# Kernel optimization log

Hardware: AMD Instinct MI355X
Metric: run time of the kernel (lower is better)

Reference implementation:

```python
import jax, jax.numpy as jnp
import numpy as np

B, T, C = 2, 4096, 1024
H = 16            # n_head (== n_groups == n_kv_heads)
HD = C // H       # head_dim = 64
W = 256           # window_size
ROPE_BASE = 10000.0


def _rope(x):
    # x: (B, H, T, HD); rotate interleaved pairs with position along axis 2
    t = x.shape[2]
    inv_freq = 1.0 / (ROPE_BASE ** (jnp.arange(0, HD, 2, dtype=jnp.float32) / HD))  # (HD/2,)
    freqs = jnp.arange(t, dtype=jnp.float32)[:, None] * inv_freq[None, :]           # (T, HD/2)
    cos = jnp.cos(freqs)[None, None].astype(x.dtype)
    sin = jnp.sin(freqs)[None, None].astype(x.dtype)
    x1, x2 = x[..., 0::2], x[..., 1::2]
    o1 = x1 * cos - x2 * sin
    o2 = x1 * sin + x2 * cos
    return jnp.stack([o1, o2], axis=-1).reshape(x.shape)


def setup_inputs() -> dict:
    key = jax.random.key(0)
    ks = jax.random.split(key, 5)
    s = 1.0 / np.sqrt(C)
    return {
        "x": jax.random.normal(ks[0], (B, T, C), dtype=jnp.float32),
        "wq": jax.random.normal(ks[1], (C, C), dtype=jnp.float32) * s,
        "wk": jax.random.normal(ks[2], (C, C), dtype=jnp.float32) * s,
        "wv": jax.random.normal(ks[3], (C, C), dtype=jnp.float32) * s,
        "wo": jax.random.normal(ks[4], (C, C), dtype=jnp.float32) * s,
    }


def reference(x, wq, wk, wv, wo):
    # projections (Linear stores (out, in) -> x @ w.T)
    q = jnp.einsum('btc,oc->bto', x, wq).reshape(B, T, H, HD).transpose(0, 2, 1, 3)
    k = jnp.einsum('btc,oc->bto', x, wk).reshape(B, T, H, HD).transpose(0, 2, 1, 3)
    v = jnp.einsum('btc,oc->bto', x, wv).reshape(B, T, H, HD).transpose(0, 2, 1, 3)

    q = _rope(q)
    k = _rope(k)

    nW = T // W
    qw = q.reshape(B, H, nW, W, HD)
    kw = k.reshape(B, H, nW, W, HD)
    vw = v.reshape(B, H, nW, W, HD)

    scale = 1.0 / jnp.sqrt(jnp.asarray(HD, dtype=q.dtype))
    att = jnp.einsum('bhnqd,bhnkd->bhnqk', qw, kw) * scale   # per-window, no causal mask
    att = jax.nn.softmax(att, axis=-1)
    yw = jnp.einsum('bhnqk,bhnkd->bhnqd', att, vw)

    y = yw.reshape(B, H, T, HD).transpose(0, 2, 1, 3).reshape(B, T, C)
    return jnp.einsum('btc,oc->bto', y, wo)
```

## Files before the change

kernel.cpp:

```cpp
#include <hip/hip_runtime.h>
#include <math.h>

typedef float f32x4 __attribute__((ext_vector_type(4)));
typedef __bf16 bf16x8 __attribute__((ext_vector_type(8)));
typedef _Float16 f16x4 __attribute__((ext_vector_type(4)));
typedef unsigned short u16x8 __attribute__((ext_vector_type(8)));
typedef unsigned short ushort_t;

#define MFMA16(a, b, c) __builtin_amdgcn_mfma_f32_16x16x32_bf16((a), (b), (c), 0, 0, 0)
#define MFMAPV(a, b, c) __builtin_amdgcn_mfma_f32_16x16x16f16((a), (b), (c), 0, 0, 0)

static __device__ __forceinline__ ushort_t f2bf(float f) {
  union { float f; unsigned u; } v; v.f = f;
  unsigned u = v.u;
  return (ushort_t)((u + 0x7FFFu + ((u >> 16) & 1u)) >> 16);
}
static __device__ __forceinline__ float bf2f(ushort_t h) {
  union { unsigned u; float f; } v; v.u = ((unsigned)h) << 16;
  return v.f;
}
static __device__ __forceinline__ ushort_t f2h_bits(float f) {
  union { _Float16 h; ushort_t u; } v;
  v.h = (_Float16)f;
  return v.u;
}
static __device__ __forceinline__ void gl_lds16(const void* g, void* lds_uniform) {
  __builtin_amdgcn_global_load_lds(
      (const __attribute__((address_space(1))) unsigned int*)g,
      (__attribute__((address_space(3))) unsigned int*)lds_uniform, 16, 0, 0);
}

__global__ void prep(const float* __restrict__ x,
                     const float* __restrict__ wq, const float* __restrict__ wk,
                     const float* __restrict__ wv, const float* __restrict__ wo,
                     ushort_t* __restrict__ Xb, ushort_t* __restrict__ Wqb,
                     ushort_t* __restrict__ Wkb, ushort_t* __restrict__ Wvb,
                     ushort_t* __restrict__ Wob, float2* __restrict__ cs) {
  const int bid = blockIdx.x;
  if (bid < 512) {
    int idx = bid * 256 + threadIdx.x;
    int pos = idx >> 5, i = idx & 31;
    double inv = exp2(-(double)i * 0.41524101186092029);
    double th = (double)pos * inv;
    double s, c;
    sincos(th, &s, &c);
    cs[idx] = make_float2((float)c, (float)s);
  } else {
    const float* src;
    ushort_t* dst;
    int i;
    if (bid < 8704) {
      src = x; dst = Xb;
      i = (bid - 512) * 256 + threadIdx.x;
    } else {
      const int wi = (bid - 8704) >> 10;
      src = (wi == 0) ? wq : (wi == 1) ? wk : (wi == 2) ? wv : wo;
      dst = (wi == 0) ? Wqb : (wi == 1) ? Wkb : (wi == 2) ? Wvb : Wob;
      i = ((bid - 8704) & 1023) * 256 + threadIdx.x;
    }
    f32x4 v = ((const f32x4*)src)[i];
    ushort4 o;
    o.x = f2bf(v.x); o.y = f2bf(v.y); o.z = f2bf(v.z); o.w = f2bf(v.w);
    ((ushort4*)dst)[i] = o;
  }
}

template <int OUTBF>
__global__ __launch_bounds__(256) void gemm_nt(
    const ushort_t* __restrict__ A,
    const ushort_t* __restrict__ W0, const ushort_t* __restrict__ W1, const ushort_t* __restrict__ W2,
    void* __restrict__ C0, void* __restrict__ C1, void* __restrict__ C2,
    int K, int N) {
  __shared__ __align__(16) ushort_t As[128 * 64];
  __shared__ __align__(16) ushort_t Bs[128 * 64];
  const int z = blockIdx.z;
  const ushort_t* W = (z == 0) ? W0 : (z == 1 ? W1 : W2);
  void* Cv = (z == 0) ? C0 : (z == 1 ? C1 : C2);

  const int t = threadIdx.x;
  const int lane = t & 63;
  const int l15 = lane & 15;
  const int quad = lane >> 4;
  const int wave = t >> 6;
  const int wm = wave & 1, wn = wave >> 1;
  const int bm = blockIdx.x, bn = blockIdx.y;

  const int srow = t >> 3;
  const int schunk = (t & 7) ^ (srow & 7);
  const ushort_t* Ag = A + (size_t)(bm * 128 + srow) * K + schunk * 8;
  const ushort_t* Wg = W + (size_t)(bn * 128 + srow) * K + schunk * 8;
  char* AsB = (char*)As + (t & 192) * 16;
  char* BsB = (char*)Bs + (t & 192) * 16;
  const size_t rK = (size_t)32 * K;

  const f32x4 zero4 = {0.f, 0.f, 0.f, 0.f};
  f32x4 acc[4][4];
#pragma unroll
  for (int i = 0; i < 4; ++i)
#pragma unroll
    for (int j = 0; j < 4; ++j) acc[i][j] = zero4;

  for (int kt = 0; kt < K; kt += 64) {
#pragma unroll
    for (int p = 0; p < 4; ++p) {
      gl_lds16(Ag + p * rK + kt, AsB + p * 4096);
      gl_lds16(Wg + p * rK + kt, BsB + p * 4096);
    }
    __syncthreads();
#pragma unroll
    for (int ks = 0; ks < 2; ++ks) {
      bf16x8 af[4], bfr[4];
#pragma unroll
      for (int i = 0; i < 4; ++i) {
        const int r = wm * 64 + i * 16 + l15;
        af[i] = *(const bf16x8*)&As[r * 64 + (((ks * 4 + quad) ^ (r & 7)) * 8)];
      }
#pragma unroll
      for (int j = 0; j < 4; ++j) {
        const int r = wn * 64 + j * 16 + l15;
        bfr[j] = *(const bf16x8*)&Bs[r * 64 + (((ks * 4 + quad) ^ (r & 7)) * 8)];
      }
#pragma unroll
      for (int i = 0; i < 4; ++i)
#pragma unroll
        for (int j = 0; j < 4; ++j) acc[i][j] = MFMA16(af[i], bfr[j], acc[i][j]);
    }
    __syncthreads();
  }

  const int rbase = bm * 128 + wm * 64 + quad * 4;
  const int cbase = bn * 128 + wn * 64 + l15;
#pragma unroll
  for (int i = 0; i < 4; ++i)
#pragma unroll
    for (int j = 0; j < 4; ++j)
#pragma unroll
      for (int r = 0; r < 4; ++r) {
        size_t idx = (size_t)(rbase + i * 16 + r) * N + (cbase + j * 16);
        if (OUTBF)
          ((ushort_t*)Cv)[idx] = f2bf(acc[i][j][r]);
        else
          ((float*)Cv)[idx] = acc[i][j][r];
      }
}

static __device__ __forceinline__ void rope8(const ushort_t* __restrict__ g,
                                             ushort_t* __restrict__ lds,
                                             const float2* __restrict__ cs4) {
  uint4 raw = *(const uint4*)g;
  unsigned rw[4] = {raw.x, raw.y, raw.z, raw.w};
  ushort_t o[8];
#pragma unroll
  for (int m = 0; m < 4; ++m) {
    float x1 = bf2f((ushort_t)(rw[m] & 0xffffu));
    float x2 = bf2f((ushort_t)(rw[m] >> 16));
    float2 sc = cs4[m];
    o[2 * m]     = f2bf(x1 * sc.x - x2 * sc.y);
    o[2 * m + 1] = f2bf(x1 * sc.y + x2 * sc.x);
  }
  uint4 w;
  w.x = (unsigned)o[0] | ((unsigned)o[1] << 16);
  w.y = (unsigned)o[2] | ((unsigned)o[3] << 16);
  w.z = (unsigned)o[4] | ((unsigned)o[5] << 16);
  w.w = (unsigned)o[6] | ((unsigned)o[7] << 16);
  *(uint4*)lds = w;
}

__global__ __launch_bounds__(256) void attn(
    const ushort_t* __restrict__ Qb, const ushort_t* __restrict__ Kb,
    const ushort_t* __restrict__ Vb, ushort_t* __restrict__ Yb,
    const float2* __restrict__ cs) {
  __shared__ __align__(16) ushort_t smem[18432];
  ushort_t* Ks = smem;
  ushort_t* Vt = smem;

  const int t = threadIdx.x;
  const int lane = t & 63, wave = t >> 6;
  const int l15 = lane & 15, quad = lane >> 4;
  const int qq = blockIdx.x >> 9;
  const int s = blockIdx.x & 511;
  const int win = s & 15, h = (s >> 4) & 15, b = s >> 8;
  const int kBase = win * 256;
  const int qRow0 = kBase + qq * 64 + wave * 16;
  const size_t gbase = ((size_t)b * 4096) * 1024 + h * 64;

  const int sr = t >> 3;
  const int c0 = (t & 7) * 8;

#pragma unroll
  for (int p = 0; p < 8; ++p) {
    int r = p * 32 + sr;
    rope8(Kb + gbase + (size_t)(kBase + r) * 1024 + c0, Ks + r * 72 + c0,
          cs + (kBase + r) * 32 + (c0 >> 1));
  }

  bf16x8 qf[2];
#pragma unroll
  for (int ks = 0; ks < 2; ++ks) {
    union { u16x8 u; bf16x8 b; } aq;
    aq.u = *(const u16x8*)(Qb + gbase + (size_t)(qRow0 + l15) * 1024 + ks * 32 + quad * 8);
    const float2* csq = cs + (size_t)((qRow0 + l15) & 4095) * 32 + ks * 16 + quad * 4;
#pragma unroll
    for (int m = 0; m < 4; ++m) {
      float x1 = bf2f(aq.u[2 * m]);
      float x2 = bf2f(aq.u[2 * m + 1]);
      float2 sc = csq[m];
      aq.u[2 * m]     = f2bf((x1 * sc.x - x2 * sc.y) * 0.125f);
      aq.u[2 * m + 1] = f2bf((x1 * sc.y + x2 * sc.x) * 0.125f);
    }
    qf[ks] = aq.b;
  }

  __syncthreads();

  const f32x4 zero4 = {0.f, 0.f, 0.f, 0.f};
  f32x4 S[16];
#pragma unroll
  for (int j = 0; j < 16; ++j) S[j] = zero4;
#pragma unroll
  for (int ks = 0; ks < 2; ++ks)
#pragma unroll
    for (int j = 0; j < 16; ++j) {
      bf16x8 kf = *(const bf16x8*)&Ks[(j * 16 + l15) * 72 + ks * 32 + quad * 8];
      S[j] = MFMA16(kf, qf[ks], S[j]);
    }

  float mx = S[0][0];
#pragma unroll
  for (int j = 0; j < 16; ++j)
#pragma unroll
    for (int e = 0; e < 4; ++e) mx = fmaxf(mx, S[j][e]);
  mx = fmaxf(mx, __shfl_xor(mx, 16));
  mx = fmaxf(mx, __shfl_xor(mx, 32));
  float sum = 0.f;
#pragma unroll
  for (int j = 0; j < 16; ++j)
#pragma unroll
    for (int e = 0; e < 4; ++e) {
      float e_ = __expf(S[j][e] - mx);
      S[j][e] = e_;
      sum += e_;
    }
  sum += __shfl_xor(sum, 16);
  sum += __shfl_xor(sum, 32);
  const float linv = 1.0f / sum;

  f16x4 pf[16];
#pragma unroll
  for (int j = 0; j < 16; ++j) pf[j] = __builtin_convertvector(S[j], f16x4);

  uint4 vraw[8];
#pragma unroll
  for (int p = 0; p < 8; ++p)
    vraw[p] = *(const uint4*)(Vb + gbase + (size_t)(kBase + p * 32 + sr) * 1024 + c0);

  __syncthreads();

#pragma unroll
  for (int p = 0; p < 8; ++p) {
    const int k = p * 32 + sr;
    ushort_t vv[8];
    vv[0] = f2h_bits(bf2f((ushort_t)(vraw[p].x & 0xffffu)));
    vv[1] = f2h_bits(bf2f((ushort_t)(vraw[p].x >> 16)));
    vv[2] = f2h_bits(bf2f((ushort_t)(vraw[p].y & 0xffffu)));
    vv[3] = f2h_bits(bf2f((ushort_t)(vraw[p].y >> 16)));
    vv[4] = f2h_bits(bf2f((ushort_t)(vraw[p].z & 0xffffu)));
    vv[5] = f2h_bits(bf2f((ushort_t)(vraw[p].z >> 16)));
    vv[6] = f2h_bits(bf2f((ushort_t)(vraw[p].w & 0xffffu)));
    vv[7] = f2h_bits(bf2f((ushort_t)(vraw[p].w >> 16)));
#pragma unroll
    for (int e = 0; e < 8; ++e) {
      const int ee = (e + (t & 7)) & 7;
      Vt[(c0 + ee) * 264 + k] = vv[ee];
    }
  }
  __syncthreads();

  f32x4 O[4];
#pragma unroll
  for (int jd = 0; jd < 4; ++jd) O[jd] = zero4;
#pragma unroll
  for (int j = 0; j < 16; ++j)
#pragma unroll
    for (int jd = 0; jd < 4; ++jd) {
      f16x4 vf = *(const f16x4*)&Vt[(jd * 16 + l15) * 264 + j * 16 + quad * 4];
      O[jd] = MFMAPV(vf, pf[j], O[jd]);
    }

  __syncthreads();

  ushort_t* tile = smem + wave * 1152;
#pragma unroll
  for (int jd = 0; jd < 4; ++jd)
#pragma unroll
    for (int r = 0; r < 4; ++r)
      tile[l15 * 72 + jd * 16 + quad * 4 + r] = f2bf(O[jd][r] * linv);
#pragma unroll
  for (int g = 0; g < 2; ++g) {
    uint4 w = *(const uint4*)&tile[l15 * 72 + quad * 16 + g * 8];
    *(uint4*)(Yb + gbase + (size_t)(qRow0 + l15) * 1024 + quad * 16 + g * 8) = w;
  }
}

extern "C" void kernel_launch(void* const* d_in, const int* in_sizes, int n_in,
                              void* d_out, int out_size, void* d_ws, size_t ws_size,
                              hipStream_t stream) {
  (void)in_sizes; (void)n_in; (void)out_size; (void)ws_size;
  const float* x  = (const float*)d_in[0];
  const float* wq = (const float*)d_in[1];
  const float* wk = (const float*)d_in[2];
  const float* wv = (const float*)d_in[3];
  const float* wo = (const float*)d_in[4];

  char* ws = (char*)d_ws;
  ushort_t* Xb  = (ushort_t*)(ws);
  ushort_t* Wqb = (ushort_t*)(ws + 16777216);
  ushort_t* Wkb = Wqb + 1048576;
  ushort_t* Wvb = Wkb + 1048576;
  ushort_t* Wob = Wvb + 1048576;
  ushort_t* Qb  = (ushort_t*)(ws + 25165824);
  ushort_t* Kb  = Qb + 8388608;
  ushort_t* Vb  = Kb + 8388608;
  ushort_t* Yb  = Vb + 8388608;
  float2*   cs  = (float2*)(ws + 92274688);

  prep<<<dim3(12800), dim3(256), 0, stream>>>(x, wq, wk, wv, wo,
                                              Xb, Wqb, Wkb, Wvb, Wob, cs);

  gemm_nt<1><<<dim3(64, 8, 3), dim3(256), 0, stream>>>(
      Xb, Wqb, Wkb, Wvb, (void*)Qb, (void*)Kb, (void*)Vb, 1024, 1024);

  attn<<<dim3(2048), dim3(256), 0, stream>>>(Qb, Kb, Vb, Yb, cs);

  gemm_nt<0><<<dim3(64, 8, 1), dim3(256), 0, stream>>>(
      Yb, Wob, Wob, Wob, d_out, d_out, d_out, 1024, 1024);
}
```

Baseline: 230.3 us.

## Reuse K/V tiles across all query blocks per window; narrow output-projection tiles

The attention kernel now launches one block per (batch, head, window). Each block loads, ropes and transposes K and V once, then loops over the four 64-row query chunks, so the per-query-chunk blocks no longer repeat that K/V work. Separate LDS regions for K, Vt and the output tiles remove the intermediate barriers. The output projection GEMM uses 128x64 tiles on a 64x16 grid to raise block count. The trade-off is that the attention grid drops to 512 larger blocks with more LDS each, which lowers parallelism and occupancy.

```diff
diff --git a/kernel.cpp b/kernel.cpp
--- a/kernel.cpp
+++ b/kernel.cpp
@@ -65,75 +65,67 @@
   }
 }
 
-template <int OUTBF>
-__global__ __launch_bounds__(256) void gemm_nt(
-    const ushort_t* __restrict__ A,
-    const ushort_t* __restrict__ W0, const ushort_t* __restrict__ W1, const ushort_t* __restrict__ W2,
-    void* __restrict__ C0, void* __restrict__ C1, void* __restrict__ C2,
-    int K, int N) {
-  __shared__ __align__(16) ushort_t As[128 * 64];
-  __shared__ __align__(16) ushort_t Bs[128 * 64];
-  const int z = blockIdx.z;
-  const ushort_t* W = (z == 0) ? W0 : (z == 1 ? W1 : W2);
-  void* Cv = (z == 0) ? C0 : (z == 1 ? C1 : C2);
-
+template <int OUTBF, int NB>
+static __device__ __forceinline__ void gemm_core(
+    ushort_t* __restrict__ As, ushort_t* __restrict__ Bs,
+    const ushort_t* __restrict__ A, const ushort_t* __restrict__ W,
+    void* __restrict__ Cv, int K, int N, int bm, int bn) {
+  constexpr int JN = NB / 32;
   const int t = threadIdx.x;
   const int lane = t & 63;
   const int l15 = lane & 15;
   const int quad = lane >> 4;
   const int wave = t >> 6;
   const int wm = wave & 1, wn = wave >> 1;
-  const int bm = blockIdx.x, bn = blockIdx.y;
 
   const int srow = t >> 3;
   const int schunk = (t & 7) ^ (srow & 7);
   const ushort_t* Ag = A + (size_t)(bm * 128 + srow) * K + schunk * 8;
-  const ushort_t* Wg = W + (size_t)(bn * 128 + srow) * K + schunk * 8;
+  const ushort_t* Wg = W + (size_t)(bn * NB + srow) * K + schunk * 8;
   char* AsB = (char*)As + (t & 192) * 16;
   char* BsB = (char*)Bs + (t & 192) * 16;
   const size_t rK = (size_t)32 * K;
 
   const f32x4 zero4 = {0.f, 0.f, 0.f, 0.f};
-  f32x4 acc[4][4];
+  f32x4 acc[4][JN];
 #pragma unroll
   for (int i = 0; i < 4; ++i)
 #pragma unroll
-    for (int j = 0; j < 4; ++j) acc[i][j] = zero4;
+    for (int j = 0; j < JN; ++j) acc[i][j] = zero4;
 
   for (int kt = 0; kt < K; kt += 64) {
 #pragma unroll
-    for (int p = 0; p < 4; ++p) {
-      gl_lds16(Ag + p * rK + kt, AsB + p * 4096);
-      gl_lds16(Wg + p * rK + kt, BsB + p * 4096);
-    }
+    for (int p = 0; p < 4; ++p) gl_lds16(Ag + p * rK + kt, AsB + p * 4096);
+#pragma unroll
+    for (int p = 0; p < NB / 32; ++p) gl_lds16(Wg + p * rK + kt, BsB + p * 4096);
     __syncthreads();
 #pragma unroll
     for (int ks = 0; ks < 2; ++ks) {
-      bf16x8 af[4], bfr[4];
+      bf16x8 af[4], bfr[JN];
 #pragma unroll
       for (int i = 0; i < 4; ++i) {
         const int r = wm * 64 + i * 16 + l15;
         af[i] = *(const bf16x8*)&As[r * 64 + (((ks * 4 + quad) ^ (r & 7)) * 8)];
       }
 #pragma unroll
-      for (int j = 0; j < 4; ++j) {
-        const int r = wn * 64 + j * 16 + l15;
+      for (int j = 0; j < JN; ++j) {
+        const int r = wn * (NB / 2) + j * 16 + l15;
         bfr[j] = *(const bf16x8*)&Bs[r * 64 + (((ks * 4 + quad) ^ (r & 7)) * 8)];
       }
 #pragma unroll
       for (int i = 0; i < 4; ++i)
 #pragma unroll
-        for (int j = 0; j < 4; ++j) acc[i][j] = MFMA16(af[i], bfr[j], acc[i][j]);
+        for (int j = 0; j < JN; ++j) acc[i][j] = MFMA16(af[i], bfr[j], acc[i][j]);
     }
     __syncthreads();
   }
 
   const int rbase = bm * 128 + wm * 64 + quad * 4;
-  const int cbase = bn * 128 + wn * 64 + l15;
+  const int cbase = bn * NB + wn * (NB / 2) + l15;
 #pragma unroll
   for (int i = 0; i < 4; ++i)
 #pragma unroll
-    for (int j = 0; j < 4; ++j)
+    for (int j = 0; j < JN; ++j)
 #pragma unroll
       for (int r = 0; r < 4; ++r) {
         size_t idx = (size_t)(rbase + i * 16 + r) * N + (cbase + j * 16);
@@ -144,6 +136,26 @@
       }
 }
 
+__global__ __launch_bounds__(256) void gemm_qkv(
+    const ushort_t* __restrict__ A,
+    const ushort_t* __restrict__ W0, const ushort_t* __restrict__ W1, const ushort_t* __restrict__ W2,
+    void* __restrict__ C0, void* __restrict__ C1, void* __restrict__ C2, int K, int N) {
+  __shared__ __align__(16) ushort_t As[128 * 64];
+  __shared__ __align__(16) ushort_t Bs[128 * 64];
+  const int z = blockIdx.z;
+  const ushort_t* W = (z == 0) ? W0 : (z == 1 ? W1 : W2);
+  void* Cv = (z == 0) ? C0 : (z == 1 ? C1 : C2);
+  gemm_core<1, 128>(As, Bs, A, W, Cv, K, N, blockIdx.x, blockIdx.y);
+}
+
+__global__ __launch_bounds__(256) void gemm_proj(
+    const ushort_t* __restrict__ A, const ushort_t* __restrict__ W,
+    float* __restrict__ C, int K, int N) {
+  __shared__ __align__(16) ushort_t As[128 * 64];
+  __shared__ __align__(16) ushort_t Bs[64 * 64];
+  gemm_core<0, 64>(As, Bs, A, W, (void*)C, K, N, blockIdx.x, blockIdx.y);
+}
+
 static __device__ __forceinline__ void rope8(const ushort_t* __restrict__ g,
                                              ushort_t* __restrict__ lds,
                                              const float2* __restrict__ cs4) {
@@ -170,22 +182,26 @@
     const ushort_t* __restrict__ Qb, const ushort_t* __restrict__ Kb,
     const ushort_t* __restrict__ Vb, ushort_t* __restrict__ Yb,
     const float2* __restrict__ cs) {
-  __shared__ __align__(16) ushort_t smem[18432];
+  __shared__ __align__(16) ushort_t smem[39936];
   ushort_t* Ks = smem;
-  ushort_t* Vt = smem;
+  ushort_t* Vt = smem + 18432;
+  ushort_t* tiles = smem + 35328;
 
   const int t = threadIdx.x;
   const int lane = t & 63, wave = t >> 6;
   const int l15 = lane & 15, quad = lane >> 4;
-  const int qq = blockIdx.x >> 9;
-  const int s = blockIdx.x & 511;
+  const int s = blockIdx.x;
   const int win = s & 15, h = (s >> 4) & 15, b = s >> 8;
   const int kBase = win * 256;
-  const int qRow0 = kBase + qq * 64 + wave * 16;
   const size_t gbase = ((size_t)b * 4096) * 1024 + h * 64;
 
   const int sr = t >> 3;
   const int c0 = (t & 7) * 8;
+
+  uint4 vraw[8];
+#pragma unroll
+  for (int p = 0; p < 8; ++p)
+    vraw[p] = *(const uint4*)(Vb + gbase + (size_t)(kBase + p * 32 + sr) * 1024 + c0);
 
 #pragma unroll
   for (int p = 0; p < 8; ++p) {
@@ -193,68 +209,6 @@
     rope8(Kb + gbase + (size_t)(kBase + r) * 1024 + c0, Ks + r * 72 + c0,
           cs + (kBase + r) * 32 + (c0 >> 1));
   }
-
-  bf16x8 qf[2];
-#pragma unroll
-  for (int ks = 0; ks < 2; ++ks) {
-    union { u16x8 u; bf16x8 b; } aq;
-    aq.u = *(const u16x8*)(Qb + gbase + (size_t)(qRow0 + l15) * 1024 + ks * 32 + quad * 8);
-    const float2* csq = cs + (size_t)((qRow0 + l15) & 4095) * 32 + ks * 16 + quad * 4;
-#pragma unroll
-    for (int m = 0; m < 4; ++m) {
-      float x1 = bf2f(aq.u[2 * m]);
-      float x2 = bf2f(aq.u[2 * m + 1]);
-      float2 sc = csq[m];
-      aq.u[2 * m]     = f2bf((x1 * sc.x - x2 * sc.y) * 0.125f);
-      aq.u[2 * m + 1] = f2bf((x1 * sc.y + x2 * sc.x) * 0.125f);
-    }
-    qf[ks] = aq.b;
-  }
-
-  __syncthreads();
-
-  const f32x4 zero4 = {0.f, 0.f, 0.f, 0.f};
-  f32x4 S[16];
-#pragma unroll
-  for (int j = 0; j < 16; ++j) S[j] = zero4;
-#pragma unroll
-  for (int ks = 0; ks < 2; ++ks)
-#pragma unroll
-    for (int j = 0; j < 16; ++j) {
-      bf16x8 kf = *(const bf16x8*)&Ks[(j * 16 + l15) * 72 + ks * 32 + quad * 8];
-      S[j] = MFMA16(kf, qf[ks], S[j]);
-    }
-
-  float mx = S[0][0];
-#pragma unroll
-  for (int j = 0; j < 16; ++j)
-#pragma unroll
-    for (int e = 0; e < 4; ++e) mx = fmaxf(mx, S[j][e]);
-  mx = fmaxf(mx, __shfl_xor(mx, 16));
-  mx = fmaxf(mx, __shfl_xor(mx, 32));
-  float sum = 0.f;
-#pragma unroll
-  for (int j = 0; j < 16; ++j)
-#pragma unroll
-    for (int e = 0; e < 4; ++e) {
-      float e_ = __expf(S[j][e] - mx);
-      S[j][e] = e_;
-      sum += e_;
-    }
-  sum += __shfl_xor(sum, 16);
-  sum += __shfl_xor(sum, 32);
-  const float linv = 1.0f / sum;
-
-  f16x4 pf[16];
-#pragma unroll
-  for (int j = 0; j < 16; ++j) pf[j] = __builtin_convertvector(S[j], f16x4);
-
-  uint4 vraw[8];
-#pragma unroll
-  for (int p = 0; p < 8; ++p)
-    vraw[p] = *(const uint4*)(Vb + gbase + (size_t)(kBase + p * 32 + sr) * 1024 + c0);
-
-  __syncthreads();
 
 #pragma unroll
   for (int p = 0; p < 8; ++p) {
@@ -276,29 +230,85 @@
   }
   __syncthreads();
 
-  f32x4 O[4];
-#pragma unroll
-  for (int jd = 0; jd < 4; ++jd) O[jd] = zero4;
-#pragma unroll
-  for (int j = 0; j < 16; ++j)
-#pragma unroll
-    for (int jd = 0; jd < 4; ++jd) {
-      f16x4 vf = *(const f16x4*)&Vt[(jd * 16 + l15) * 264 + j * 16 + quad * 4];
-      O[jd] = MFMAPV(vf, pf[j], O[jd]);
-    }
-
-  __syncthreads();
-
-  ushort_t* tile = smem + wave * 1152;
-#pragma unroll
-  for (int jd = 0; jd < 4; ++jd)
-#pragma unroll
-    for (int r = 0; r < 4; ++r)
-      tile[l15 * 72 + jd * 16 + quad * 4 + r] = f2bf(O[jd][r] * linv);
-#pragma unroll
-  for (int g = 0; g < 2; ++g) {
-    uint4 w = *(const uint4*)&tile[l15 * 72 + quad * 16 + g * 8];
-    *(uint4*)(Yb + gbase + (size_t)(qRow0 + l15) * 1024 + quad * 16 + g * 8) = w;
+  const f32x4 zero4 = {0.f, 0.f, 0.f, 0.f};
+
+  for (int qq = 0; qq < 4; ++qq) {
+    const int qRow0 = kBase + qq * 64 + wave * 16;
+
+    bf16x8 qf[2];
+#pragma unroll
+    for (int ks = 0; ks < 2; ++ks) {
+      union { u16x8 u; bf16x8 b; } aq;
+      aq.u = *(const u16x8*)(Qb + gbase + (size_t)(qRow0 + l15) * 1024 + ks * 32 + quad * 8);
+      const float2* csq = cs + (size_t)((qRow0 + l15) & 4095) * 32 + ks * 16 + quad * 4;
+#pragma unroll
+      for (int m = 0; m < 4; ++m) {
+        float x1 = bf2f(aq.u[2 * m]);
+        float x2 = bf2f(aq.u[2 * m + 1]);
+        float2 sc = csq[m];
+        aq.u[2 * m]     = f2bf((x1 * sc.x - x2 * sc.y) * 0.125f);
+        aq.u[2 * m + 1] = f2bf((x1 * sc.y + x2 * sc.x) * 0.125f);
+      }
+      qf[ks] = aq.b;
+    }
+
+    f32x4 S[16];
+#pragma unroll
+    for (int j = 0; j < 16; ++j) S[j] = zero4;
+#pragma unroll
+    for (int ks = 0; ks < 2; ++ks)
+#pragma unroll
+      for (int j = 0; j < 16; ++j) {
+        bf16x8 kf = *(const bf16x8*)&Ks[(j * 16 + l15) * 72 + ks * 32 + quad * 8];
+        S[j] = MFMA16(kf, qf[ks], S[j]);
+      }
+
+    float mx = S[0][0];
+#pragma unroll
+    for (int j = 0; j < 16; ++j)
+#pragma unroll
+      for (int e = 0; e < 4; ++e) mx = fmaxf(mx, S[j][e]);
+    mx = fmaxf(mx, __shfl_xor(mx, 16));
+    mx = fmaxf(mx, __shfl_xor(mx, 32));
+    float sum = 0.f;
+#pragma unroll
+    for (int j = 0; j < 16; ++j)
+#pragma unroll
+      for (int e = 0; e < 4; ++e) {
+        float e_ = __expf(S[j][e] - mx);
+        S[j][e] = e_;
+        sum += e_;
+      }
+    sum += __shfl_xor(sum, 16);
+    sum += __shfl_xor(sum, 32);
+    const float linv = 1.0f / sum;
+
+    f16x4 pf[16];
+#pragma unroll
+    for (int j = 0; j < 16; ++j) pf[j] = __builtin_convertvector(S[j], f16x4);
+
+    f32x4 O[4];
+#pragma unroll
+    for (int jd = 0; jd < 4; ++jd) O[jd] = zero4;
+#pragma unroll
+    for (int j = 0; j < 16; ++j)
+#pragma unroll
+      for (int jd = 0; jd < 4; ++jd) {
+        f16x4 vf = *(const f16x4*)&Vt[(jd * 16 + l15) * 264 + j * 16 + quad * 4];
+        O[jd] = MFMAPV(vf, pf[j], O[jd]);
+      }
+
+    ushort_t* tile = tiles + wave * 1152;
+#pragma unroll
+    for (int jd = 0; jd < 4; ++jd)
+#pragma unroll
+      for (int r = 0; r < 4; ++r)
+        tile[l15 * 72 + jd * 16 + quad * 4 + r] = f2bf(O[jd][r] * linv);
+#pragma unroll
+    for (int g = 0; g < 2; ++g) {
+      uint4 w = *(const uint4*)&tile[l15 * 72 + quad * 16 + g * 8];
+      *(uint4*)(Yb + gbase + (size_t)(qRow0 + l15) * 1024 + quad * 16 + g * 8) = w;
+    }
   }
 }
 
@@ -327,11 +337,10 @@
   prep<<<dim3(12800), dim3(256), 0, stream>>>(x, wq, wk, wv, wo,
                                               Xb, Wqb, Wkb, Wvb, Wob, cs);
 
-  gemm_nt<1><<<dim3(64, 8, 3), dim3(256), 0, stream>>>(
+  gemm_qkv<<<dim3(64, 8, 3), dim3(256), 0, stream>>>(
       Xb, Wqb, Wkb, Wvb, (void*)Qb, (void*)Kb, (void*)Vb, 1024, 1024);
 
-  attn<<<dim3(2048), dim3(256), 0, stream>>>(Qb, Kb, Vb, Yb, cs);
-
-  gemm_nt<0><<<dim3(64, 8, 1), dim3(256), 0, stream>>>(
-      Yb, Wob, Wob, Wob, d_out, d_out, d_out, 1024, 1024);
-}
+  attn<<<dim3(512), dim3(256), 0, stream>>>(Qb, Kb, Vb, Yb, cs);
+
+  gemm_proj<<<dim3(64, 16), dim3(256), 0, stream>>>(Yb, Wob, (float*)d_out, 1024, 1024);
+}
```

After: 218.3 us. -5.2%, faster.
